# Kernel tuning notes

Measured on AMD Instinct MI355X. Metric: run time of the kernel, lower is better.

Reference implementation:

```python
import jax, jax.numpy as jnp
import numpy as np

B, N, T, HID, HOPS = 128, 32, 50, 128, 8


def setup_inputs() -> dict:
    key = jax.random.key(0)
    k1, k2, k3, k4 = jax.random.split(key, 4)
    return {
        "node_rnn_output": jax.random.normal(k1, (B, T, HID), dtype=jnp.float32),
        "neigh_rnn_output": jax.random.normal(k2, (B, N, T, HID), dtype=jnp.float32),
        "neighbors_number": jnp.ones((B,), dtype=jnp.int32),
        "W": jax.random.normal(k3, (HOPS, HID), dtype=jnp.float32) * 0.05,
        "b": jax.random.normal(k4, (HOPS,), dtype=jnp.float32) * 0.05,
    }


def reference(node_rnn_output, neigh_rnn_output, neighbors_number, W, b):
    Bb, Tt, Hd = node_rnn_output.shape
    Nn = neigh_rnn_output.shape[1]
    # neigh_rnn_output.view(B, -1, hidden)  -> [B, N*T, H]
    neigh_r = neigh_rnn_output.reshape(Bb, Nn * Tt, Hd)
    # node_rnn_output.repeat(1, N, 1)      -> tile along time axis N times
    node_tiled = jnp.tile(node_rnn_output, (1, Nn, 1))  # [B, N*T, H]
    # elementwise guide + tiny linear projection to attention hops
    Hprod = neigh_r * node_tiled                         # [B, N*T, H]
    s1 = jnp.einsum('bnh,ah->bna', Hprod, W) + b          # [B, N*T, hops]
    # original scales every sample by sqrt(neighbors_number[0])
    scale = neighbors_number[0].astype(jnp.float32) ** 0.5
    s1 = jnp.swapaxes(s1, 1, 2) / scale                   # [B, hops, N*T]
    BA = jax.nn.softmax(s1, axis=-1)                      # [B, hops, N*T]
    # BW built from A.data (detached) in the original
    BW = jax.lax.stop_gradient(BA).sum(axis=1).reshape(Bb, Nn, Tt)
    return (BW, BA, neigh_r)
```

## Files before the change

### kernel.cpp

```cpp
#include <hip/hip_runtime.h>
#include <cmath>

namespace {

typedef float f32x4 __attribute__((ext_vector_type(4)));

constexpr int Bb   = 128;
constexpr int Nn   = 32;
constexpr int Tt   = 50;
constexpr int Hh   = 128;
constexpr int HOPS = 8;
constexpr int NT   = Nn * Tt;
constexpr int PPT  = 5;
constexpr int POS_PER_BLOCK = 16 * PPT;
constexpr int CHUNKS = NT / POS_PER_BLOCK;

__global__ __launch_bounds__(256) void ga_s1_copy(
    const float* __restrict__ node,
    const float* __restrict__ neigh,
    const int*   __restrict__ nn,
    const float* __restrict__ W,
    const float* __restrict__ bias,
    float* __restrict__ s1T,
    float* __restrict__ neigh_r)
{
    const int lane16 = threadIdx.x & 15;
    const int group  = threadIdx.x >> 4;
    const int chunk  = blockIdx.x % CHUNKS;
    const int b      = blockIdx.x / CHUNKS;

    const float rscale = rsqrtf((float)nn[0]);

    f32x4 w0[HOPS], w1[HOPS];
    #pragma unroll
    for (int a = 0; a < HOPS; ++a) {
        const f32x4* wp = reinterpret_cast<const f32x4*>(W + a * Hh + lane16 * 8);
        w0[a] = wp[0];
        w1[a] = wp[1];
    }
    const float bl = bias[lane16 >> 1];

    const int pos0 = chunk * POS_PER_BLOCK + group;
    const size_t base = ((size_t)b * NT + pos0) * Hh + lane16 * 8;

    f32x4 nb[PPT][2];
    #pragma unroll
    for (int p = 0; p < PPT; ++p) {
        const f32x4* np = reinterpret_cast<const f32x4*>(neigh + base + (size_t)p * 16 * Hh);
        nb[p][0] = np[0];
        nb[p][1] = np[1];
    }
    #pragma unroll
    for (int p = 0; p < PPT; ++p) {
        f32x4* cp = reinterpret_cast<f32x4*>(neigh_r + base + (size_t)p * 16 * Hh);
        cp[0] = nb[p][0];
        cp[1] = nb[p][1];
    }

    #pragma unroll
    for (int p = 0; p < PPT; ++p) {
        const int pos = pos0 + p * 16;
        const int t   = pos % Tt;
        const f32x4* dp = reinterpret_cast<const f32x4*>(node + ((size_t)b * Tt + t) * Hh + lane16 * 8);
        const f32x4 pr0 = nb[p][0] * dp[0];
        const f32x4 pr1 = nb[p][1] * dp[1];

        float acc[HOPS];
        #pragma unroll
        for (int a = 0; a < HOPS; ++a) {
            acc[a] = pr0[0] * w0[a][0] + pr0[1] * w0[a][1] + pr0[2] * w0[a][2] + pr0[3] * w0[a][3]
                   + pr1[0] * w1[a][0] + pr1[1] * w1[a][1] + pr1[2] * w1[a][2] + pr1[3] * w1[a][3];
        }

        const bool h8 = (lane16 & 8) != 0;
        float r[4];
        #pragma unroll
        for (int k = 0; k < 4; ++k) {
            float send = h8 ? acc[k] : acc[k + 4];
            r[k] = (h8 ? acc[k + 4] : acc[k]) + __shfl_xor(send, 8, 64);
        }
        const bool h4 = (lane16 & 4) != 0;
        float s2[2];
        #pragma unroll
        for (int k = 0; k < 2; ++k) {
            float send = h4 ? r[k] : r[k + 2];
            s2[k] = (h4 ? r[k + 2] : r[k]) + __shfl_xor(send, 4, 64);
        }
        const bool h2 = (lane16 & 2) != 0;
        float send3 = h2 ? s2[0] : s2[1];
        float u = (h2 ? s2[1] : s2[0]) + __shfl_xor(send3, 2, 64);
        u += __shfl_xor(u, 1, 64);

        if (!(lane16 & 1)) {
            const int k = lane16 >> 1;
            s1T[((size_t)b * HOPS + k) * NT + pos] = (u + bl) * rscale;
        }
    }
}

__global__ __launch_bounds__(256) void ga_softmax_rows(float* __restrict__ BA)
{
    const int a = blockIdx.x & 7;
    const int b = blockIdx.x >> 3;
    float* row = BA + ((size_t)b * HOPS + a) * NT;

    const int tid  = threadIdx.x;
    const int wv   = tid >> 6;
    const int lane = tid & 63;

    float v[7];
    #pragma unroll
    for (int k = 0; k < 7; ++k) {
        const int nt = tid + k * 256;
        v[k] = (nt < NT) ? row[nt] : -INFINITY;
    }

    __shared__ float red[4];

    float m = v[0];
    #pragma unroll
    for (int k = 1; k < 7; ++k) m = fmaxf(m, v[k]);
    #pragma unroll
    for (int off = 32; off >= 1; off >>= 1) m = fmaxf(m, __shfl_xor(m, off, 64));
    if (lane == 0) red[wv] = m;
    __syncthreads();
    m = fmaxf(fmaxf(red[0], red[1]), fmaxf(red[2], red[3]));
    __syncthreads();

    float e[7];
    float s = 0.f;
    #pragma unroll
    for (int k = 0; k < 7; ++k) {
        const int nt = tid + k * 256;
        e[k] = (nt < NT) ? __expf(v[k] - m) : 0.f;
        s += e[k];
    }
    #pragma unroll
    for (int off = 32; off >= 1; off >>= 1) s += __shfl_xor(s, off, 64);
    if (lane == 0) red[wv] = s;
    __syncthreads();
    const float inv = 1.0f / (red[0] + red[1] + red[2] + red[3]);

    #pragma unroll
    for (int k = 0; k < 7; ++k) {
        const int nt = tid + k * 256;
        if (nt < NT) row[nt] = e[k] * inv;
    }
}

__global__ __launch_bounds__(256) void ga_bw(const float* __restrict__ BA,
                                             float* __restrict__ BW)
{
    const int b  = blockIdx.y;
    const int nt = blockIdx.x * 256 + threadIdx.x;
    if (nt >= NT) return;
    const float* base = BA + (size_t)b * HOPS * NT + nt;
    float s = 0.f;
    #pragma unroll
    for (int a = 0; a < HOPS; ++a) s += base[a * NT];
    BW[(size_t)b * NT + nt] = s;
}

}

extern "C" void kernel_launch(void* const* d_in, const int* in_sizes, int n_in,
                              void* d_out, int out_size, void* d_ws, size_t ws_size,
                              hipStream_t stream) {
    const float* node  = (const float*)d_in[0];
    const float* neigh = (const float*)d_in[1];
    const int*   nn    = (const int*)d_in[2];
    const float* W     = (const float*)d_in[3];
    const float* bias  = (const float*)d_in[4];

    float* out     = (float*)d_out;
    float* BA      = out + Bb * NT;
    float* neigh_r = BA + Bb * HOPS * NT;

    ga_s1_copy<<<dim3(Bb * CHUNKS), dim3(256), 0, stream>>>(node, neigh, nn, W, bias, BA, neigh_r);
    ga_softmax_rows<<<dim3(Bb * HOPS), dim3(256), 0, stream>>>(BA);
    ga_bw<<<dim3((NT + 255) / 256, Bb), dim3(256), 0, stream>>>(BA, out);
}
```

Measured before the change: 52.59 us.

## Fuse softmax and hop-sum into one per-batch kernel using shared memory

```diff
diff --git a/kernel.cpp b/kernel.cpp
--- a/kernel.cpp
+++ b/kernel.cpp
@@ -98,67 +98,68 @@
     }
 }
 
-__global__ __launch_bounds__(256) void ga_softmax_rows(float* __restrict__ BA)
+__global__ __launch_bounds__(1024) void ga_softmax_bw(float* __restrict__ out)
 {
-    const int a = blockIdx.x & 7;
-    const int b = blockIdx.x >> 3;
-    float* row = BA + ((size_t)b * HOPS + a) * NT;
+    float* BW = out;
+    float* BA = out + Bb * NT;
+    const int b  = blockIdx.x;
+    const int tl = threadIdx.x & 127;
+    const int r  = threadIdx.x >> 7;
+    const int wave = threadIdx.x >> 6;
+    const int lane = threadIdx.x & 63;
 
-    const int tid  = threadIdx.x;
-    const int wv   = tid >> 6;
-    const int lane = tid & 63;
+    float* row = BA + ((size_t)b * HOPS + r) * NT;
 
-    float v[7];
+    float v[13];
     #pragma unroll
-    for (int k = 0; k < 7; ++k) {
-        const int nt = tid + k * 256;
+    for (int k = 0; k < 13; ++k) {
+        const int nt = k * 128 + tl;
         v[k] = (nt < NT) ? row[nt] : -INFINITY;
     }
 
-    __shared__ float red[4];
+    __shared__ float redm[16], reds[16];
+    __shared__ float sP[HOPS][NT + 4];
 
     float m = v[0];
     #pragma unroll
-    for (int k = 1; k < 7; ++k) m = fmaxf(m, v[k]);
+    for (int k = 1; k < 13; ++k) m = fmaxf(m, v[k]);
     #pragma unroll
     for (int off = 32; off >= 1; off >>= 1) m = fmaxf(m, __shfl_xor(m, off, 64));
-    if (lane == 0) red[wv] = m;
+    if (lane == 0) redm[wave] = m;
     __syncthreads();
-    m = fmaxf(fmaxf(red[0], red[1]), fmaxf(red[2], red[3]));
-    __syncthreads();
+    m = fmaxf(redm[r * 2], redm[r * 2 + 1]);
 
-    float e[7];
+    float e[13];
     float s = 0.f;
     #pragma unroll
-    for (int k = 0; k < 7; ++k) {
-        const int nt = tid + k * 256;
+    for (int k = 0; k < 13; ++k) {
+        const int nt = k * 128 + tl;
         e[k] = (nt < NT) ? __expf(v[k] - m) : 0.f;
         s += e[k];
     }
     #pragma unroll
     for (int off = 32; off >= 1; off >>= 1) s += __shfl_xor(s, off, 64);
-    if (lane == 0) red[wv] = s;
+    if (lane == 0) reds[wave] = s;
     __syncthreads();
-    const float inv = 1.0f / (red[0] + red[1] + red[2] + red[3]);
+    const float inv = 1.0f / (reds[r * 2] + reds[r * 2 + 1]);
 
     #pragma unroll
-    for (int k = 0; k < 7; ++k) {
-        const int nt = tid + k * 256;
-        if (nt < NT) row[nt] = e[k] * inv;
+    for (int k = 0; k < 13; ++k) {
+        const int nt = k * 128 + tl;
+        if (nt < NT) {
+            const float p = e[k] * inv;
+            row[nt] = p;
+            sP[r][nt] = p;
+        }
     }
-}
+    __syncthreads();
 
-__global__ __launch_bounds__(256) void ga_bw(const float* __restrict__ BA,
-                                             float* __restrict__ BW)
-{
-    const int b  = blockIdx.y;
-    const int nt = blockIdx.x * 256 + threadIdx.x;
-    if (nt >= NT) return;
-    const float* base = BA + (size_t)b * HOPS * NT + nt;
-    float s = 0.f;
-    #pragma unroll
-    for (int a = 0; a < HOPS; ++a) s += base[a * NT];
-    BW[(size_t)b * NT + nt] = s;
+    for (int nt = threadIdx.x; nt < NT; nt += 1024) {
+        float ssum = 0.f;
+        #pragma unroll
+        for (int a = 0; a < HOPS; ++a) ssum += sP[a][nt];
+        BW[(size_t)b * NT + nt] = ssum;
+    }
 }
 
 }
@@ -177,6 +178,5 @@
     float* neigh_r = BA + Bb * HOPS * NT;
 
     ga_s1_copy<<<dim3(Bb * CHUNKS), dim3(256), 0, stream>>>(node, neigh, nn, W, bias, BA, neigh_r);
-    ga_softmax_rows<<<dim3(Bb * HOPS), dim3(256), 0, stream>>>(BA);
-    ga_bw<<<dim3((NT + 255) / 256, Bb), dim3(256), 0, stream>>>(BA, out);
+    ga_softmax_bw<<<dim3(Bb), dim3(1024), 0, stream>>>(out);
 }
```

Measured after the change: 50.79 us. -3.4%, faster.
